# Optimization experiments

Measured on AMD Instinct MI355X. Metric: run time of the kernel, lower is better.

## Reference

```python
import jax, jax.numpy as jnp
import numpy as np

PRECISION_BITS = 6
NOISE_SCALE = 1.0 / (2 ** (2 * PRECISION_BITS))  # 1/4096, as in call()


def setup_inputs() -> dict:
    key = jax.random.key(0)
    k1, k2, k3, k4, k5 = jax.random.split(key, 5)
    B, D_IN, UNITS = 4096, 4096, 4096
    x = jax.random.normal(k1, (B, D_IN), dtype=jnp.float32)
    kernel = jax.random.normal(k2, (D_IN, UNITS), dtype=jnp.float32) * 0.02
    # per-unit fitted Gaussian params (stats.norm.fit of the convolved error PMF)
    noise_mean = jax.random.normal(k3, (UNITS,), dtype=jnp.float32)
    noise_std = jax.random.uniform(k4, (UNITS,), dtype=jnp.float32)
    # pre-drawn standard-normal variates replacing scipy rvs() for determinism
    noise_eps = jax.random.normal(k5, (B, UNITS), dtype=jnp.float32)
    return {"x": x, "kernel": kernel, "noise_mean": noise_mean,
            "noise_std": noise_std, "noise_eps": noise_eps}


def reference(x, kernel, noise_mean, noise_std, noise_eps):
    # outputs = x @ kernel  ([B, D] @ [D, U] -> [B, U])
    outputs = jnp.matmul(x, kernel)
    # per-unit Gaussian noise: norm(loc=mean[u], scale=std[u]).rvs(B) / 2**(2*pb)
    noise = (noise_mean[None, :] + noise_std[None, :] * noise_eps) * NOISE_SCALE
    outputs = outputs + noise
    # activation is None in this configuration
    return outputs
```

## Files before the change

kernel.cpp:

```cpp
#include <hip/hip_runtime.h>
#include <hip/hip_bf16.h>
#include <stdint.h>

typedef short bf16x8 __attribute__((ext_vector_type(8)));
typedef float f32x4 __attribute__((ext_vector_type(4)));
typedef unsigned short u16x8 __attribute__((ext_vector_type(8)));

#define GLB(p)  ((__attribute__((address_space(1))) void*)(uintptr_t)(p))
#define LDSP(p) ((__attribute__((address_space(3))) void*)(p))

#define BM 128
#define BN 128
#define BK 32

__device__ __forceinline__ void bf16_split(float x, unsigned short& h, unsigned short& l) {
  unsigned u = __float_as_uint(x);
  unsigned hb = (u + 0x7FFFu + ((u >> 16) & 1u)) >> 16;
  h = (unsigned short)hb;
  float d = x - __uint_as_float(hb << 16);
  unsigned u2 = __float_as_uint(d);
  l = (unsigned short)((u2 + 0x7FFFu + ((u2 >> 16) & 1u)) >> 16);
}

__global__ void convert_split_k(const float* __restrict__ in,
                                unsigned short* __restrict__ hi,
                                unsigned short* __restrict__ lo, long n) {
  long i = ((long)blockIdx.x * blockDim.x + threadIdx.x) * 8;
  if (i + 8 > n) return;
  float v[8];
  *(float4*)(&v[0]) = *(const float4*)(in + i);
  *(float4*)(&v[4]) = *(const float4*)(in + i + 4);
  u16x8 vh, vl;
#pragma unroll
  for (int e = 0; e < 8; ++e) {
    unsigned short h, l;
    bf16_split(v[e], h, l);
    vh[e] = h; vl[e] = l;
  }
  *(u16x8*)(hi + i) = vh;
  *(u16x8*)(lo + i) = vl;
}

__global__ void transpose_split_k(const float* __restrict__ in,
                                  unsigned short* __restrict__ hiT,
                                  unsigned short* __restrict__ loT,
                                  int Dk, int U) {
  const int ublocks = U >> 8;
  const int ub = blockIdx.x % ublocks;
  const int db = blockIdx.x / ublocks;
  const int u  = (ub << 8) + threadIdx.x;
  const int d0 = db * 32;
  unsigned short h[32], l[32];
#pragma unroll
  for (int i = 0; i < 32; ++i) {
    float x = in[(long)(d0 + i) * U + u];
    bf16_split(x, h[i], l[i]);
  }
  u16x8* ph = (u16x8*)(hiT + (long)u * Dk + d0);
  u16x8* pl = (u16x8*)(loT + (long)u * Dk + d0);
#pragma unroll
  for (int q = 0; q < 4; ++q) {
    u16x8 vh, vl;
#pragma unroll
    for (int e = 0; e < 8; ++e) { vh[e] = h[q * 8 + e]; vl[e] = l[q * 8 + e]; }
    ph[q] = vh;
    pl[q] = vl;
  }
}

__global__ __launch_bounds__(256) void gemm_bf16x3(
    const unsigned short* __restrict__ Ahi, const unsigned short* __restrict__ Alo,
    const unsigned short* __restrict__ Bhi, const unsigned short* __restrict__ Blo,
    const float* __restrict__ nmean, const float* __restrict__ nstd,
    const float* __restrict__ eps, float* __restrict__ out,
    int M, int N, int K)
{
  __shared__ unsigned short sAhi[BM * BK], sAlo[BM * BK];
  __shared__ unsigned short sBhi[BN * BK], sBlo[BN * BK];

  const int tid  = threadIdx.x;
  const int wid  = tid >> 6;
  const int lane = tid & 63;
  const int l15  = lane & 15;
  const int kg   = lane >> 4;

  const int nbm = M / BM, nbn = N / BN, nwg = nbm * nbn;
  const int bid = blockIdx.x;
  const int swz = ((nwg & 7) == 0) ? ((bid & 7) * (nwg >> 3) + (bid >> 3)) : bid;
  const int bm = swz % nbm, bn = swz / nbm;

  const int wm = wid >> 1, wn = wid & 1;
  const int rowA0 = bm * BM;
  const int rowB0 = bn * BN;

  f32x4 acc[4][4];
#pragma unroll
  for (int i = 0; i < 4; ++i)
#pragma unroll
    for (int j = 0; j < 4; ++j) acc[i][j] = (f32x4)0.0f;

  for (int kt = 0; kt < K; kt += BK) {
#pragma unroll
    for (int j = 0; j < 2; ++j) {
      const int c = wid * 2 + j;
      const int m = c * 16 + (lane >> 2);
      const int s = lane & 3;
      const int g = s ^ ((m >> 1) & 3);
      const long koff = (long)kt + g * 8;
      const int lofs = c * 512;
      __builtin_amdgcn_global_load_lds(GLB(Ahi + (long)(rowA0 + m) * K + koff), LDSP(&sAhi[lofs]), 16, 0, 0);
      __builtin_amdgcn_global_load_lds(GLB(Alo + (long)(rowA0 + m) * K + koff), LDSP(&sAlo[lofs]), 16, 0, 0);
      __builtin_amdgcn_global_load_lds(GLB(Bhi + (long)(rowB0 + m) * K + koff), LDSP(&sBhi[lofs]), 16, 0, 0);
      __builtin_amdgcn_global_load_lds(GLB(Blo + (long)(rowB0 + m) * K + koff), LDSP(&sBlo[lofs]), 16, 0, 0);
    }
    __syncthreads();

    bf16x8 ah[4], al[4], bh[4], bl[4];
#pragma unroll
    for (int f = 0; f < 4; ++f) {
      const int ma = wm * 64 + f * 16 + l15;
      const int oa = ma * BK + ((kg ^ ((ma >> 1) & 3)) * 8);
      ah[f] = *(const bf16x8*)&sAhi[oa];
      al[f] = *(const bf16x8*)&sAlo[oa];
      const int mb = wn * 64 + f * 16 + l15;
      const int ob = mb * BK + ((kg ^ ((mb >> 1) & 3)) * 8);
      bh[f] = *(const bf16x8*)&sBhi[ob];
      bl[f] = *(const bf16x8*)&sBlo[ob];
    }

#pragma unroll
    for (int i = 0; i < 4; ++i)
#pragma unroll
      for (int j = 0; j < 4; ++j)
        acc[i][j] = __builtin_amdgcn_mfma_f32_16x16x32_bf16(ah[i], bh[j], acc[i][j], 0, 0, 0);
#pragma unroll
    for (int i = 0; i < 4; ++i)
#pragma unroll
      for (int j = 0; j < 4; ++j)
        acc[i][j] = __builtin_amdgcn_mfma_f32_16x16x32_bf16(ah[i], bl[j], acc[i][j], 0, 0, 0);
#pragma unroll
    for (int i = 0; i < 4; ++i)
#pragma unroll
      for (int j = 0; j < 4; ++j)
        acc[i][j] = __builtin_amdgcn_mfma_f32_16x16x32_bf16(al[i], bh[j], acc[i][j], 0, 0, 0);
    __syncthreads();
  }

  const float NS = 2.44140625e-4f;
  const int r0 = rowA0 + wm * 64;
  const int c0 = rowB0 + wn * 64;
#pragma unroll
  for (int i = 0; i < 4; ++i)
#pragma unroll
    for (int j = 0; j < 4; ++j) {
      const int col = c0 + j * 16 + l15;
      const float mn = nmean[col];
      const float sd = nstd[col];
#pragma unroll
      for (int r = 0; r < 4; ++r) {
        const int row = r0 + i * 16 + kg * 4 + r;
        const long o = (long)row * N + col;
        out[o] = acc[i][j][r] + (mn + sd * eps[o]) * NS;
      }
    }
}

__global__ __launch_bounds__(1024) void fb_gemm(
    const float* __restrict__ A, const float* __restrict__ B,
    const float* __restrict__ nmean, const float* __restrict__ nstd,
    const float* __restrict__ eps, float* __restrict__ out,
    int M, int N, int K) {
  __shared__ float sA[32][33];
  __shared__ float sB[32][33];
  const int tx = threadIdx.x & 31, ty = threadIdx.x >> 5;
  const int row = blockIdx.y * 32 + ty;
  const int col = blockIdx.x * 32 + tx;
  float acc = 0.f;
  for (int kt = 0; kt < K; kt += 32) {
    sA[ty][tx] = A[(long)row * K + kt + tx];
    sB[ty][tx] = B[(long)(kt + ty) * N + col];
    __syncthreads();
#pragma unroll
    for (int k = 0; k < 32; ++k) acc += sA[ty][k] * sB[k][tx];
    __syncthreads();
  }
  const long o = (long)row * N + col;
  out[o] = acc + (nmean[col] + nstd[col] * eps[o]) * 2.44140625e-4f;
}

extern "C" void kernel_launch(void* const* d_in, const int* in_sizes, int n_in,
                              void* d_out, int out_size, void* d_ws, size_t ws_size,
                              hipStream_t stream) {
  (void)n_in; (void)out_size;
  const float* x     = (const float*)d_in[0];
  const float* w     = (const float*)d_in[1];
  const float* nmean = (const float*)d_in[2];
  const float* nstd  = (const float*)d_in[3];
  const float* eps   = (const float*)d_in[4];
  float* out = (float*)d_out;

  const int U  = in_sizes[2];
  const int Dk = in_sizes[1] / U;
  const int Bm = in_sizes[0] / Dk;

  const size_t elemsA = (size_t)Bm * Dk;
  const size_t elemsB = (size_t)Dk * U;
  const size_t need = 2 * (elemsA + elemsB) * sizeof(unsigned short);

  const bool ok = (ws_size >= need) &&
                  (Bm % BM == 0) && (U % BN == 0) && (Dk % BK == 0) &&
                  (U % 256 == 0) && (Dk % 32 == 0) && ((elemsA % 8) == 0);

  if (ok) {
    unsigned short* Ahi  = (unsigned short*)d_ws;
    unsigned short* Alo  = Ahi + elemsA;
    unsigned short* BhiT = Alo + elemsA;
    unsigned short* BloT = BhiT + elemsB;
    const long nA = (long)elemsA;
    const int gridA = (int)((nA / 8 + 255) / 256);
    convert_split_k<<<gridA, 256, 0, stream>>>(x, Ahi, Alo, nA);
    transpose_split_k<<<(U >> 8) * (Dk / 32), 256, 0, stream>>>(w, BhiT, BloT, Dk, U);
    gemm_bf16x3<<<(Bm / BM) * (U / BN), 256, 0, stream>>>(Ahi, Alo, BhiT, BloT,
                                                          nmean, nstd, eps, out, Bm, U, Dk);
  } else {
    dim3 g(U / 32, Bm / 32);
    fb_gemm<<<g, 1024, 0, stream>>>(x, w, nmean, nstd, eps, out, Bm, U, Dk);
  }
}
```

Measured before the change: 643.4 us.

## Rewrite bf16x3 GEMM as 256x256 double-buffered 8-wave pipelined kernel

Replaces the 128x128, 4-wave, single-buffered bf16x3 GEMM with a 256x256 tile, 8-wave (512-thread) kernel. LDS is double-buffered, and the next K-tile's hi/lo A/B loads are interleaved with six MFMA phases separated by barriers, with setprio raised around the MFMA blocks. The aim is to hide global-to-LDS latency and raise arithmetic intensity per loaded byte. In exchange it uses much more LDS (128KB) and far more accumulator registers, so occupancy drops. The grid also shrinks to 256 workgroups, which may underfill the GPU.

```diff
diff --git a/kernel.cpp b/kernel.cpp
--- a/kernel.cpp
+++ b/kernel.cpp
@@ -8,10 +8,6 @@
 
 #define GLB(p)  ((__attribute__((address_space(1))) void*)(uintptr_t)(p))
 #define LDSP(p) ((__attribute__((address_space(3))) void*)(p))
-
-#define BM 128
-#define BN 128
-#define BK 32
 
 __device__ __forceinline__ void bf16_split(float x, unsigned short& h, unsigned short& l) {
   unsigned u = __float_as_uint(x);
@@ -68,98 +64,131 @@
   }
 }
 
-__global__ __launch_bounds__(256) void gemm_bf16x3(
+#define BARRIER0 __builtin_amdgcn_s_barrier()
+#define WAIT_LGKM0 do { asm volatile("s_waitcnt lgkmcnt(0)" ::: "memory"); \
+                        __builtin_amdgcn_sched_barrier(0); } while (0)
+#define WAIT_VM0 asm volatile("s_waitcnt vmcnt(0)" ::: "memory")
+
+#define MFMA_BLOCK(IB) do { \
+  __builtin_amdgcn_s_setprio(1); \
+  _Pragma("unroll") for (int i_ = 0; i_ < 4; ++i_) \
+  _Pragma("unroll") for (int j_ = 0; j_ < 4; ++j_) \
+    acc[(IB) + i_][j_] = __builtin_amdgcn_mfma_f32_16x16x32_bf16(aF[i_], bF[j_], acc[(IB) + i_][j_], 0, 0, 0); \
+  __builtin_amdgcn_s_setprio(0); } while (0)
+
+#define RD_A(HL, HALF) do { \
+  _Pragma("unroll") for (int f_ = 0; f_ < 4; ++f_) \
+    aF[f_] = *(const bf16x8*)&sA[c][HL][wm * 4096 + (HALF) * 2048 + f_ * 512 + foff]; } while (0)
+
+#define RD_B(HL) do { \
+  _Pragma("unroll") for (int f_ = 0; f_ < 4; ++f_) \
+    bF[f_] = *(const bf16x8*)&sB[c][HL][wn * 2048 + f_ * 512 + foff]; } while (0)
+
+#define STAGE2(GSRC, LBASE, KOFF) do { \
+  __builtin_amdgcn_global_load_lds(GLB((GSRC) + so0 + (KOFF)), LDSP((LBASE) + (wid << 9)), 16, 0, 0); \
+  __builtin_amdgcn_global_load_lds(GLB((GSRC) + so1 + (KOFF)), LDSP((LBASE) + 4096 + (wid << 9)), 16, 0, 0); } while (0)
+
+__global__ __launch_bounds__(512, 2) void gemm_bf16x3_8p(
     const unsigned short* __restrict__ Ahi, const unsigned short* __restrict__ Alo,
     const unsigned short* __restrict__ Bhi, const unsigned short* __restrict__ Blo,
     const float* __restrict__ nmean, const float* __restrict__ nstd,
     const float* __restrict__ eps, float* __restrict__ out,
     int M, int N, int K)
 {
-  __shared__ unsigned short sAhi[BM * BK], sAlo[BM * BK];
-  __shared__ unsigned short sBhi[BN * BK], sBlo[BN * BK];
+  __shared__ __align__(16) unsigned short sA[2][2][256 * 32];
+  __shared__ __align__(16) unsigned short sB[2][2][256 * 32];
 
   const int tid  = threadIdx.x;
   const int wid  = tid >> 6;
   const int lane = tid & 63;
   const int l15  = lane & 15;
   const int kg   = lane >> 4;
-
-  const int nbm = M / BM, nbn = N / BN, nwg = nbm * nbn;
+  const int wm   = wid >> 2;
+  const int wn   = wid & 3;
+
+  const int nbm = M >> 8, nbn = N >> 8, nwg = nbm * nbn;
   const int bid = blockIdx.x;
   const int swz = ((nwg & 7) == 0) ? ((bid & 7) * (nwg >> 3) + (bid >> 3)) : bid;
   const int bm = swz % nbm, bn = swz / nbm;
-
-  const int wm = wid >> 1, wn = wid & 1;
-  const int rowA0 = bm * BM;
-  const int rowB0 = bn * BN;
-
-  f32x4 acc[4][4];
-#pragma unroll
-  for (int i = 0; i < 4; ++i)
+  const long rowA0 = (long)bm << 8;
+  const long rowB0 = (long)bn << 8;
+
+  const unsigned short* gAh = Ahi + rowA0 * K;
+  const unsigned short* gAl = Alo + rowA0 * K;
+  const unsigned short* gBh = Bhi + rowB0 * K;
+  const unsigned short* gBl = Blo + rowB0 * K;
+
+  const int e0 = tid, e1 = tid + 512;
+  const int r0 = e0 >> 2, r1 = e1 >> 2;
+  const long so0 = (long)r0 * K + (long)(((e0 & 3) ^ ((r0 >> 1) & 3)) << 3);
+  const long so1 = (long)r1 * K + (long)(((e1 & 3) ^ ((r1 >> 1) & 3)) << 3);
+
+  const int foff = l15 * 32 + ((kg ^ ((l15 >> 1) & 3)) << 3);
+
+  f32x4 acc[8][4];
+#pragma unroll
+  for (int i = 0; i < 8; ++i)
 #pragma unroll
     for (int j = 0; j < 4; ++j) acc[i][j] = (f32x4)0.0f;
 
-  for (int kt = 0; kt < K; kt += BK) {
-#pragma unroll
-    for (int j = 0; j < 2; ++j) {
-      const int c = wid * 2 + j;
-      const int m = c * 16 + (lane >> 2);
-      const int s = lane & 3;
-      const int g = s ^ ((m >> 1) & 3);
-      const long koff = (long)kt + g * 8;
-      const int lofs = c * 512;
-      __builtin_amdgcn_global_load_lds(GLB(Ahi + (long)(rowA0 + m) * K + koff), LDSP(&sAhi[lofs]), 16, 0, 0);
-      __builtin_amdgcn_global_load_lds(GLB(Alo + (long)(rowA0 + m) * K + koff), LDSP(&sAlo[lofs]), 16, 0, 0);
-      __builtin_amdgcn_global_load_lds(GLB(Bhi + (long)(rowB0 + m) * K + koff), LDSP(&sBhi[lofs]), 16, 0, 0);
-      __builtin_amdgcn_global_load_lds(GLB(Blo + (long)(rowB0 + m) * K + koff), LDSP(&sBlo[lofs]), 16, 0, 0);
-    }
-    __syncthreads();
-
-    bf16x8 ah[4], al[4], bh[4], bl[4];
-#pragma unroll
-    for (int f = 0; f < 4; ++f) {
-      const int ma = wm * 64 + f * 16 + l15;
-      const int oa = ma * BK + ((kg ^ ((ma >> 1) & 3)) * 8);
-      ah[f] = *(const bf16x8*)&sAhi[oa];
-      al[f] = *(const bf16x8*)&sAlo[oa];
-      const int mb = wn * 64 + f * 16 + l15;
-      const int ob = mb * BK + ((kg ^ ((mb >> 1) & 3)) * 8);
-      bh[f] = *(const bf16x8*)&sBhi[ob];
-      bl[f] = *(const bf16x8*)&sBlo[ob];
-    }
-
-#pragma unroll
-    for (int i = 0; i < 4; ++i)
-#pragma unroll
-      for (int j = 0; j < 4; ++j)
-        acc[i][j] = __builtin_amdgcn_mfma_f32_16x16x32_bf16(ah[i], bh[j], acc[i][j], 0, 0, 0);
-#pragma unroll
-    for (int i = 0; i < 4; ++i)
-#pragma unroll
-      for (int j = 0; j < 4; ++j)
-        acc[i][j] = __builtin_amdgcn_mfma_f32_16x16x32_bf16(ah[i], bl[j], acc[i][j], 0, 0, 0);
-#pragma unroll
-    for (int i = 0; i < 4; ++i)
-#pragma unroll
-      for (int j = 0; j < 4; ++j)
-        acc[i][j] = __builtin_amdgcn_mfma_f32_16x16x32_bf16(al[i], bh[j], acc[i][j], 0, 0, 0);
-    __syncthreads();
+  const int nt = K >> 5;
+
+  STAGE2(gAh, &sA[0][0][0], 0);
+  STAGE2(gAl, &sA[0][1][0], 0);
+  STAGE2(gBh, &sB[0][0][0], 0);
+  STAGE2(gBl, &sB[0][1][0], 0);
+  WAIT_VM0;
+  BARRIER0;
+
+  for (int t = 0; t < nt; ++t) {
+    const int c = t & 1;
+    const long KOFF = (long)(t + 1) << 5;
+    const bool pf = (t + 1 < nt);
+    unsigned short* nAh = &sA[c ^ 1][0][0];
+    unsigned short* nAl = &sA[c ^ 1][1][0];
+    unsigned short* nBh = &sB[c ^ 1][0][0];
+    unsigned short* nBl = &sB[c ^ 1][1][0];
+    bf16x8 aF[4], bF[4];
+
+    RD_A(0, 0); RD_B(0);
+    if (pf) STAGE2(gAh, nAh, KOFF);
+    BARRIER0; WAIT_LGKM0; MFMA_BLOCK(0); BARRIER0;
+
+    RD_A(0, 1);
+    if (pf) STAGE2(gAl, nAl, KOFF);
+    BARRIER0; WAIT_LGKM0; MFMA_BLOCK(4); BARRIER0;
+
+    RD_A(0, 0); RD_B(1);
+    if (pf) STAGE2(gBh, nBh, KOFF);
+    BARRIER0; WAIT_LGKM0; MFMA_BLOCK(0); BARRIER0;
+
+    RD_A(0, 1);
+    if (pf) STAGE2(gBl, nBl, KOFF);
+    BARRIER0; WAIT_LGKM0; MFMA_BLOCK(4); BARRIER0;
+
+    RD_A(1, 0); RD_B(0);
+    BARRIER0; WAIT_LGKM0; MFMA_BLOCK(0); BARRIER0;
+
+    RD_A(1, 1);
+    BARRIER0; WAIT_LGKM0; MFMA_BLOCK(4);
+    WAIT_VM0;
+    BARRIER0;
   }
 
   const float NS = 2.44140625e-4f;
-  const int r0 = rowA0 + wm * 64;
-  const int c0 = rowB0 + wn * 64;
-#pragma unroll
-  for (int i = 0; i < 4; ++i)
+  const long r0o = rowA0 + wm * 128;
+  const long c0o = rowB0 + wn * 64;
+#pragma unroll
+  for (int i = 0; i < 8; ++i)
 #pragma unroll
     for (int j = 0; j < 4; ++j) {
-      const int col = c0 + j * 16 + l15;
+      const long col = c0o + j * 16 + l15;
       const float mn = nmean[col];
       const float sd = nstd[col];
 #pragma unroll
       for (int r = 0; r < 4; ++r) {
-        const int row = r0 + i * 16 + kg * 4 + r;
-        const long o = (long)row * N + col;
+        const long row = r0o + i * 16 + kg * 4 + r;
+        const long o = row * N + col;
         out[o] = acc[i][j][r] + (mn + sd * eps[o]) * NS;
       }
     }
@@ -208,8 +237,8 @@
   const size_t need = 2 * (elemsA + elemsB) * sizeof(unsigned short);
 
   const bool ok = (ws_size >= need) &&
-                  (Bm % BM == 0) && (U % BN == 0) && (Dk % BK == 0) &&
-                  (U % 256 == 0) && (Dk % 32 == 0) && ((elemsA % 8) == 0);
+                  (Bm % 256 == 0) && (U % 256 == 0) && (Dk % 32 == 0) &&
+                  ((elemsA % 8) == 0);
 
   if (ok) {
     unsigned short* Ahi  = (unsigned short*)d_ws;
@@ -220,8 +249,9 @@
     const int gridA = (int)((nA / 8 + 255) / 256);
     convert_split_k<<<gridA, 256, 0, stream>>>(x, Ahi, Alo, nA);
     transpose_split_k<<<(U >> 8) * (Dk / 32), 256, 0, stream>>>(w, BhiT, BloT, Dk, U);
-    gemm_bf16x3<<<(Bm / BM) * (U / BN), 256, 0, stream>>>(Ahi, Alo, BhiT, BloT,
-                                                          nmean, nstd, eps, out, Bm, U, Dk);
+    const int nwg = (Bm >> 8) * (U >> 8);
+    gemm_bf16x3_8p<<<nwg, 512, 0, stream>>>(Ahi, Alo, BhiT, BloT,
+                                            nmean, nstd, eps, out, Bm, U, Dk);
   } else {
     dim3 g(U / 32, Bm / 32);
     fb_gemm<<<g, 1024, 0, stream>>>(x, w, nmean, nstd, eps, out, Bm, U, Dk);
```

Measured after the change: 568.9 us. -11.6%, faster.
